# Kernel optimization log

Measured on AMD Instinct MI355X. Metric: run time of the kernel, lower is better.

## Reference

```python
import jax, jax.numpy as jnp
import numpy as np

N_NODES = 50000
N_EDGES = 800000
VOCAB = 15000
IN_FEATS = 128
HIDDEN = 32
HEADS = 4
N_GRAPHS = 64
NEG_SLOPE = 0.2


def setup_inputs() -> dict:
    key = jax.random.key(0)
    ks = jax.random.split(key, 16)
    word_ids = jax.random.randint(ks[0], (N_NODES,), 0, VOCAB)
    edge_src = jax.random.randint(ks[1], (N_EDGES,), 0, N_NODES)
    edge_dst = jax.random.randint(ks[2], (N_EDGES,), 0, N_NODES)
    node_graph_id = jnp.sort(jax.random.randint(ks[3], (N_NODES,), 0, N_GRAPHS))
    y_data = jax.random.uniform(ks[4], (N_GRAPHS,))
    word_embeds = jax.random.normal(ks[5], (VOCAB, IN_FEATS)) * 0.02
    W0 = jax.random.normal(ks[6], (IN_FEATS, HEADS * HIDDEN)) * (1.0 / np.sqrt(IN_FEATS))
    al0 = jax.random.normal(ks[7], (HEADS, HIDDEN)) * 0.1
    ar0 = jax.random.normal(ks[8], (HEADS, HIDDEN)) * 0.1
    W1 = jax.random.normal(ks[9], (HEADS * HIDDEN, HEADS * HIDDEN)) * (1.0 / np.sqrt(HEADS * HIDDEN))
    al1 = jax.random.normal(ks[10], (HEADS, HIDDEN)) * 0.1
    ar1 = jax.random.normal(ks[11], (HEADS, HIDDEN)) * 0.1
    out_w = jax.random.normal(ks[12], (HEADS * HIDDEN, 1)) * (1.0 / np.sqrt(HEADS * HIDDEN))
    out_b = jnp.zeros((1,))
    return {"word_ids": word_ids, "edge_src": edge_src, "edge_dst": edge_dst,
            "node_graph_id": node_graph_id, "y_data": y_data,
            "word_embeds": word_embeds, "W0": W0, "al0": al0, "ar0": ar0,
            "W1": W1, "al1": al1, "ar1": ar1, "out_w": out_w, "out_b": out_b}


def gat_layer(h, src, dst, W, al, ar):
    # h: [N, Fin] -> feat: [N, H, D]
    feat = (h @ W).reshape(N_NODES, HEADS, HIDDEN)
    el = (feat * al[None]).sum(-1)  # [N, H]
    er = (feat * ar[None]).sum(-1)  # [N, H]
    e = jax.nn.leaky_relu(el[src] + er[dst], NEG_SLOPE)  # [E, H]
    # segment softmax over incoming edges of each dst node
    m = jax.ops.segment_max(e, dst, num_segments=N_NODES)
    m = jnp.where(jnp.isfinite(m), m, 0.0)
    ex = jnp.exp(e - m[dst])
    denom = jax.ops.segment_sum(ex, dst, num_segments=N_NODES)
    alpha = ex / (denom[dst] + 1e-10)  # [E, H]
    msg = feat[src] * alpha[:, :, None]  # [E, H, D]
    out = jax.ops.segment_sum(msg, dst, num_segments=N_NODES)  # [N, H, D]
    return jax.nn.elu(out).reshape(N_NODES, HEADS * HIDDEN)


def reference(word_ids, edge_src, edge_dst, node_graph_id, y_data,
              word_embeds, W0, al0, ar0, W1, al1, ar1, out_w, out_b):
    h = word_embeds[word_ids]  # [N, IN_FEATS]
    h = gat_layer(h, edge_src, edge_dst, W0, al0, ar0)
    h = gat_layer(h, edge_src, edge_dst, W1, al1, ar1)
    # per-graph max pooling over nodes
    pooled = jax.ops.segment_max(h, node_graph_id, num_segments=N_GRAPHS)
    pooled = jnp.where(jnp.isfinite(pooled), pooled, 0.0)  # guard empty graphs
    logits = (pooled @ out_w + out_b).reshape(-1)  # [G]
    # BCE with logits (stable)
    loss = jnp.mean(jnp.maximum(logits, 0.0) - logits * y_data
                    + jnp.log1p(jnp.exp(-jnp.abs(logits))))
    y_pred = jax.nn.sigmoid(logits)[:, None]
    return (loss, y_pred)
```

## Files before the change

### kernel.cpp

```cpp
#include <hip/hip_runtime.h>
#include <math.h>

#define N_NODES 50000
#define N_EDGES 800000
#define HEADS 4
#define N_GRAPHS 64
#define NEG_SLOPE 0.2f
#define LOG2E 1.4426950408889634f
#define SCAN_NB 196
#define POOL_CHUNK 50
#define POOL_NB 1000
#define FEAT_NB 782
#define EDGE_Q 200000
#define EDGE_NB 782

typedef __attribute__((ext_vector_type(8))) short bf16x8;
typedef __attribute__((ext_vector_type(4))) float f32x4;

__device__ __forceinline__ unsigned fkey(float f) {
    unsigned u = __float_as_uint(f);
    return (u & 0x80000000u) ? ~u : (u | 0x80000000u);
}
__device__ __forceinline__ float kval(unsigned k) {
    unsigned u = (k & 0x80000000u) ? (k & 0x7FFFFFFFu) : ~k;
    return __uint_as_float(u);
}

__device__ __forceinline__ unsigned short f2bf(float f) {
    unsigned u = __float_as_uint(f);
    u += 0x7FFFu + ((u >> 16) & 1u);
    return (unsigned short)(u >> 16);
}
__device__ __forceinline__ unsigned pack_bf2(float a, float b) {
    return (unsigned)f2bf(a) | ((unsigned)f2bf(b) << 16);
}

__device__ __forceinline__ float elu_fast(float o) {
    float e = exp2f(o * LOG2E) - 1.f;
    return o > 0.f ? o : e;
}


__global__ void hist_kernel(const int* __restrict__ dst, int* __restrict__ deg,
                            int* __restrict__ rank) {
    int i = blockIdx.x * 256 + threadIdx.x;
    if (i >= EDGE_Q) return;
    int e0 = i, e1 = i + EDGE_Q, e2 = i + 2 * EDGE_Q, e3 = i + 3 * EDGE_Q;
    int d0 = dst[e0], d1 = dst[e1], d2 = dst[e2], d3 = dst[e3];
    int r0 = atomicAdd(&deg[d0], 1);
    int r1 = atomicAdd(&deg[d1], 1);
    int r2 = atomicAdd(&deg[d2], 1);
    int r3 = atomicAdd(&deg[d3], 1);
    rank[e0] = r0; rank[e1] = r1; rank[e2] = r2; rank[e3] = r3;
}

__global__ void partial_kernel(const int* __restrict__ deg, int* __restrict__ partial) {
    int t = threadIdx.x, b = blockIdx.x;
    int i = b * 256 + t;
    int v = (i < N_NODES) ? deg[i] : 0;
    #pragma unroll
    for (int off = 1; off < 64; off <<= 1) v += __shfl_xor(v, off, 64);
    __shared__ int wsum[4];
    if ((t & 63) == 0) wsum[t >> 6] = v;
    __syncthreads();
    if (t == 0) partial[b] = wsum[0] + wsum[1] + wsum[2] + wsum[3];
}

__global__ void csr_offsets_kernel(const int* __restrict__ deg, const int* __restrict__ partial,
                                   int* __restrict__ row_start) {
    __shared__ int sb[SCAN_NB];
    __shared__ int wsumA[4];
    __shared__ int wsumB[4];
    int t = threadIdx.x, b = blockIdx.x;
    int lane = t & 63, w = t >> 6;
    {
        int v = (t < SCAN_NB) ? partial[t] : 0;
        int incl = v;
        #pragma unroll
        for (int off = 1; off < 64; off <<= 1) {
            int u = __shfl_up(incl, off, 64);
            if (lane >= off) incl += u;
        }
        if (lane == 63) wsumA[w] = incl;
        __syncthreads();
        int woff = 0;
        #pragma unroll
        for (int k = 0; k < 4; ++k) if (k < w) woff += wsumA[k];
        if (t < SCAN_NB) sb[t] = woff + incl - v;
        __syncthreads();
    }
    int i = b * 256 + t;
    int v = (i < N_NODES) ? deg[i] : 0;
    int incl = v;
    #pragma unroll
    for (int off = 1; off < 64; off <<= 1) {
        int u = __shfl_up(incl, off, 64);
        if (lane >= off) incl += u;
    }
    if (lane == 63) wsumB[w] = incl;
    __syncthreads();
    int woff = sb[b];
    #pragma unroll
    for (int k = 0; k < 4; ++k) if (k < w) woff += wsumB[k];
    int excl = woff + incl - v;
    if (i < N_NODES) row_start[i] = excl;
    else if (i == N_NODES) row_start[i] = excl;
}

__device__ __forceinline__ void scatter_body(int bid, const int* __restrict__ src,
                                             const int* __restrict__ dst,
                                             const int* __restrict__ rank,
                                             const int* __restrict__ row_start,
                                             int* __restrict__ csr_src) {
    int i = bid * 256 + threadIdx.x;
    if (i >= EDGE_Q) return;
    int e0 = i, e1 = i + EDGE_Q, e2 = i + 2 * EDGE_Q, e3 = i + 3 * EDGE_Q;
    int d0 = dst[e0], d1 = dst[e1], d2 = dst[e2], d3 = dst[e3];
    int k0 = rank[e0], k1 = rank[e1], k2 = rank[e2], k3 = rank[e3];
    int s0 = src[e0], s1 = src[e1], s2 = src[e2], s3 = src[e3];
    csr_src[row_start[d0] + k0] = s0;
    csr_src[row_start[d1] + k1] = s1;
    csr_src[row_start[d2] + k2] = s2;
    csr_src[row_start[d3] + k3] = s3;
}


__device__ __forceinline__ void wfrag_body(const float* __restrict__ W,
                                           unsigned* __restrict__ wf, int slot) {
    int f = slot >> 6, l = slot & 63;
    int n = l & 15, q = l >> 4;
    int ct = f >> 2, kq = f & 3;
    int col = 16 * ct + n;
    int k0 = 32 * kq + 8 * q;
    uint4 o;
    o.x = pack_bf2(W[(k0 + 0) * 128 + col], W[(k0 + 1) * 128 + col]);
    o.y = pack_bf2(W[(k0 + 2) * 128 + col], W[(k0 + 3) * 128 + col]);
    o.z = pack_bf2(W[(k0 + 4) * 128 + col], W[(k0 + 5) * 128 + col]);
    o.w = pack_bf2(W[(k0 + 6) * 128 + col], W[(k0 + 7) * 128 + col]);
    ((uint4*)wf)[slot] = o;
}

__global__ void prep_kernel(const float* __restrict__ W0, const float* __restrict__ W1,
                            unsigned* __restrict__ wf0, unsigned* __restrict__ wf1,
                            int* __restrict__ deg, unsigned* __restrict__ pkeys) {
    int b = blockIdx.x, t = threadIdx.x;
    if (b < 8) {
        wfrag_body(W0, wf0, b * 256 + t);
    } else if (b < 16) {
        wfrag_body(W1, wf1, (b - 8) * 256 + t);
    } else if (b < 16 + SCAN_NB) {
        int i = (b - 16) * 256 + t;
        if (i < N_NODES) deg[i] = 0;
    } else {
        int i = (b - 16 - SCAN_NB) * 256 + t;
        if (i < N_GRAPHS * 128) pkeys[i] = 0;
    }
}

template<int IN_BF16>
__device__ __forceinline__ void feat_body(int bid, const void* __restrict__ hin,
                                          const int* __restrict__ wid,
                                          const unsigned* __restrict__ wf,
                                          const float* __restrict__ al,
                                          const float* __restrict__ ar,
                                          unsigned* __restrict__ featb,
                                          float* __restrict__ el, float* __restrict__ er) {
    __shared__ unsigned hl[64 * 68];
    int t = threadIdx.x;
    int n0 = bid * 64;
    if (IN_BF16) {
        const uint4* hb4 = (const uint4*)hin;
        #pragma unroll
        for (int r = 0; r < 4; ++r) {
            int i = t + 256 * r;
            int n = i >> 4, q = i & 15;
            uint4 v = {0u, 0u, 0u, 0u};
            int gn = n0 + n;
            if (gn < N_NODES) v = hb4[(size_t)gn * 16 + q];
            *(uint4*)&hl[n * 68 + q * 4] = v;
        }
    } else {
        const float4* h4 = (const float4*)hin;
        #pragma unroll
        for (int r = 0; r < 8; ++r) {
            int i = t + 256 * r;
            int n = i >> 5, q4 = i & 31;
            float4 v = {0.f, 0.f, 0.f, 0.f};
            int gn = n0 + n;
            if (gn < N_NODES) {
                int row = wid ? wid[gn] : gn;
                v = h4[(size_t)row * 32 + q4];
            }
            hl[n * 68 + q4 * 2]     = pack_bf2(v.x, v.y);
            hl[n * 68 + q4 * 2 + 1] = pack_bf2(v.z, v.w);
        }
    }
    __syncthreads();
    int w = t >> 6, lane = t & 63;
    int col = lane & 15, quad = lane >> 4;
    int nbase = n0 + 16 * w;
    bf16x8 afr[4];
    #pragma unroll
    for (int kq = 0; kq < 4; ++kq)
        afr[kq] = *(const bf16x8*)&hl[(16 * w + col) * 68 + 16 * kq + 4 * quad];
    f32x4 acc[8];
    #pragma unroll
    for (int ct = 0; ct < 8; ++ct) acc[ct] = (f32x4){0.f, 0.f, 0.f, 0.f};
    const uint4* wf4 = (const uint4*)wf;
    #pragma unroll
    for (int ct = 0; ct < 8; ++ct) {
        #pragma unroll
        for (int kq = 0; kq < 4; ++kq) {
            uint4 braw = wf4[(ct * 4 + kq) * 64 + lane];
            bf16x8 bfr = *(const bf16x8*)&braw;
            acc[ct] = __builtin_amdgcn_mfma_f32_16x16x32_bf16(afr[kq], bfr, acc[ct], 0, 0, 0);
        }
    }
    #pragma unroll
    for (int ct = 0; ct < 8; ++ct) {
        #pragma unroll
        for (int reg = 0; reg < 4; ++reg) {
            float v = acc[ct][reg];
            float pv = __shfl_xor(v, 1, 64);
            int node = nbase + quad * 4 + reg;
            if (!(col & 1) && node < N_NODES)
                featb[(size_t)node * 64 + ct * 8 + (col >> 1)] = pack_bf2(v, pv);
        }
    }
    float alv[8], arv[8];
    #pragma unroll
    for (int ct = 0; ct < 8; ++ct) {
        alv[ct] = al[ct * 16 + col];
        arv[ct] = ar[ct * 16 + col];
    }
    #pragma unroll
    for (int reg = 0; reg < 4; ++reg) {
        int node = nbase + quad * 4 + reg;
        #pragma unroll
        for (int hd = 0; hd < 4; ++hd) {
            float pl = acc[2 * hd][reg] * alv[2 * hd] + acc[2 * hd + 1][reg] * alv[2 * hd + 1];
            float pr = acc[2 * hd][reg] * arv[2 * hd] + acc[2 * hd + 1][reg] * arv[2 * hd + 1];
            #pragma unroll
            for (int off = 1; off < 16; off <<= 1) {
                pl += __shfl_xor(pl, off, 64);
                pr += __shfl_xor(pr, off, 64);
            }
            if (col == hd && node < N_NODES) {
                el[node * 4 + hd] = pl * LOG2E;
                er[node * 4 + hd] = pr * LOG2E;
            }
        }
    }
}

template<int IN_BF16>
__global__ __launch_bounds__(256)
void feat_kernel_t(const void* __restrict__ hin, const int* __restrict__ wid,
                   const unsigned* __restrict__ wf,
                   const float* __restrict__ al, const float* __restrict__ ar,
                   unsigned* __restrict__ featb, float* __restrict__ el,
                   float* __restrict__ er) {
    feat_body<IN_BF16>(blockIdx.x, hin, wid, wf, al, ar, featb, el, er);
}

__global__ __launch_bounds__(256)
void scatter_feat0_kernel(const int* __restrict__ src, const int* __restrict__ dst,
                          const int* __restrict__ rank, const int* __restrict__ row_start,
                          int* __restrict__ csr_src,
                          const float* __restrict__ emb, const int* __restrict__ wid,
                          const unsigned* __restrict__ wf0,
                          const float* __restrict__ al0, const float* __restrict__ ar0,
                          unsigned* __restrict__ featb, float* __restrict__ el,
                          float* __restrict__ er) {
    if (blockIdx.x < EDGE_NB) {
        scatter_body(blockIdx.x, src, dst, rank, row_start, csr_src);
    } else {
        feat_body<0>(blockIdx.x - EDGE_NB, emb, wid, wf0, al0, ar0, featb, el, er);
    }
}

template<int OUT_BF16>
__global__ void gat_aggregate_t(const int* __restrict__ row_start, const int* __restrict__ csr_src,
                                const unsigned* __restrict__ featb, const float* __restrict__ el,
                                const float* __restrict__ er, float* __restrict__ houtf,
                                unsigned* __restrict__ houtb) {
    int lane = threadIdx.x & 63;
    int d = blockIdx.x * 4 + (threadIdx.x >> 6);
    int beg = row_start[d], end = row_start[d + 1];
    int eg = lane >> 4;
    int li = lane & 15;
    int hc = li >> 2;
    float er_h = er[d * 4 + hc];
    float a0 = 0.f, a1 = 0.f, a2 = 0.f, a3 = 0.f;
    float a4 = 0.f, a5 = 0.f, a6 = 0.f, a7 = 0.f;
    float dsum = 0.f;
    int b8 = beg + ((end - beg) & ~7);
    for (int base = beg; base < b8; base += 8) {
        int ea = base + eg, eb = base + 4 + eg;
        int sa = csr_src[ea];
        int sb = csr_src[eb];
        float la = el[sa * 4 + hc];
        float lb = el[sb * 4 + hc];
        uint4 pa = *(const uint4*)(featb + (size_t)sa * 64 + li * 4);
        uint4 pb = *(const uint4*)(featb + (size_t)sb * 64 + li * 4);
        float va = la + er_h; va = fmaxf(va, NEG_SLOPE * va);
        float vb = lb + er_h; vb = fmaxf(vb, NEG_SLOPE * vb);
        float xa = exp2f(va), xb = exp2f(vb);
        dsum += xa + xb;
        a0 += __uint_as_float(pa.x << 16) * xa;
        a1 += __uint_as_float(pa.x & 0xFFFF0000u) * xa;
        a2 += __uint_as_float(pa.y << 16) * xa;
        a3 += __uint_as_float(pa.y & 0xFFFF0000u) * xa;
        a4 += __uint_as_float(pa.z << 16) * xa;
        a5 += __uint_as_float(pa.z & 0xFFFF0000u) * xa;
        a6 += __uint_as_float(pa.w << 16) * xa;
        a7 += __uint_as_float(pa.w & 0xFFFF0000u) * xa;
        a0 += __uint_as_float(pb.x << 16) * xb;
        a1 += __uint_as_float(pb.x & 0xFFFF0000u) * xb;
        a2 += __uint_as_float(pb.y << 16) * xb;
        a3 += __uint_as_float(pb.y & 0xFFFF0000u) * xb;
        a4 += __uint_as_float(pb.z << 16) * xb;
        a5 += __uint_as_float(pb.z & 0xFFFF0000u) * xb;
        a6 += __uint_as_float(pb.w << 16) * xb;
        a7 += __uint_as_float(pb.w & 0xFFFF0000u) * xb;
    }
    for (int ee = b8 + eg; ee < end; ee += 4) {
        int s = csr_src[ee];
        float lv = el[s * 4 + hc];
        uint4 pv = *(const uint4*)(featb + (size_t)s * 64 + li * 4);
        float v = lv + er_h; v = fmaxf(v, NEG_SLOPE * v);
        float x = exp2f(v);
        dsum += x;
        a0 += __uint_as_float(pv.x << 16) * x;
        a1 += __uint_as_float(pv.x & 0xFFFF0000u) * x;
        a2 += __uint_as_float(pv.y << 16) * x;
        a3 += __uint_as_float(pv.y & 0xFFFF0000u) * x;
        a4 += __uint_as_float(pv.z << 16) * x;
        a5 += __uint_as_float(pv.z & 0xFFFF0000u) * x;
        a6 += __uint_as_float(pv.w << 16) * x;
        a7 += __uint_as_float(pv.w & 0xFFFF0000u) * x;
    }
    #pragma unroll
    for (int off = 16; off < 64; off <<= 1) {
        a0 += __shfl_xor(a0, off, 64);
        a1 += __shfl_xor(a1, off, 64);
        a2 += __shfl_xor(a2, off, 64);
        a3 += __shfl_xor(a3, off, 64);
        a4 += __shfl_xor(a4, off, 64);
        a5 += __shfl_xor(a5, off, 64);
        a6 += __shfl_xor(a6, off, 64);
        a7 += __shfl_xor(a7, off, 64);
        dsum += __shfl_xor(dsum, off, 64);
    }
    if (eg == 0) {
        float inv = 1.f / (dsum + 1e-10f);
        float o0 = elu_fast(a0 * inv), o1 = elu_fast(a1 * inv);
        float o2 = elu_fast(a2 * inv), o3 = elu_fast(a3 * inv);
        float o4 = elu_fast(a4 * inv), o5 = elu_fast(a5 * inv);
        float o6 = elu_fast(a6 * inv), o7 = elu_fast(a7 * inv);
        if (OUT_BF16) {
            uint4 wv;
            wv.x = pack_bf2(o0, o1);
            wv.y = pack_bf2(o2, o3);
            wv.z = pack_bf2(o4, o5);
            wv.w = pack_bf2(o6, o7);
            ((uint4*)(houtb + (size_t)d * 64))[li] = wv;
        } else {
            float4* op = (float4*)(houtf + (size_t)d * 128);
            float4 w0 = {o0, o1, o2, o3};
            float4 w1 = {o4, o5, o6, o7};
            op[li * 2] = w0;
            op[li * 2 + 1] = w1;
        }
    }
}


__global__ void pool_kernel(const int* __restrict__ gid, const float* __restrict__ h,
                            unsigned* __restrict__ pkeys) {
    int t = threadIdx.x;
    int c = t & 127;
    int par = t >> 7;
    int n0 = blockIdx.x * POOL_CHUNK;
    float m = 0.f;
    int cur_g = -1;
    for (int n = n0 + par; n < n0 + POOL_CHUNK; n += 2) {
        int g = gid[n];
        if (g != cur_g) {
            if (cur_g >= 0) atomicMax(&pkeys[cur_g * 128 + c], fkey(m));
            cur_g = g;
            m = -3.0e38f;
        }
        m = fmaxf(m, h[(size_t)n * 128 + c]);
    }
    if (cur_g >= 0) atomicMax(&pkeys[cur_g * 128 + c], fkey(m));
}

__global__ void logits_final_kernel(const unsigned* __restrict__ pkeys,
                                    const float* __restrict__ w, const float* __restrict__ bptr,
                                    const float* __restrict__ y, float* __restrict__ out) {
    __shared__ float slog[N_GRAPHS];
    int t = threadIdx.x;
    int wv = t >> 6, lane = t & 63;
    float b = bptr[0];
    #pragma unroll
    for (int k = 0; k < 16; ++k) {
        int g = wv * 16 + k;
        float sum = 0.f;
        #pragma unroll
        for (int c0 = 0; c0 < 128; c0 += 64) {
            int c = c0 + lane;
            unsigned kk = pkeys[g * 128 + c];
            float v = (kk == 0u) ? 0.f : kval(kk);
            sum += v * w[c];
        }
        #pragma unroll
        for (int off = 32; off; off >>= 1) sum += __shfl_down(sum, off, 64);
        if (lane == 0) slog[g] = sum + b;
    }
    __syncthreads();
    if (t < N_GRAPHS) {
        float l = slog[t];
        float term = fmaxf(l, 0.f) - l * y[t] + log1pf(expf(-fabsf(l)));
        float s = term;
        #pragma unroll
        for (int off = 32; off; off >>= 1) s += __shfl_down(s, off, 64);
        out[1 + t] = 1.f / (1.f + expf(-l));
        if (t == 0) out[0] = s * (1.f / 64.f);
    }
}

extern "C" void kernel_launch(void* const* d_in, const int* in_sizes, int n_in,
                              void* d_out, int out_size, void* d_ws, size_t ws_size,
                              hipStream_t stream) {
    const int* word_ids  = (const int*)d_in[0];
    const int* esrc      = (const int*)d_in[1];
    const int* edst      = (const int*)d_in[2];
    const int* gid       = (const int*)d_in[3];
    const float* y_data  = (const float*)d_in[4];
    const float* emb     = (const float*)d_in[5];
    const float* W0      = (const float*)d_in[6];
    const float* al0     = (const float*)d_in[7];
    const float* ar0     = (const float*)d_in[8];
    const float* W1      = (const float*)d_in[9];
    const float* al1     = (const float*)d_in[10];
    const float* ar1     = (const float*)d_in[11];
    const float* out_w   = (const float*)d_in[12];
    const float* out_b   = (const float*)d_in[13];
    float* out = (float*)d_out;

    float* ws = (float*)d_ws;
    unsigned* featb  = (unsigned*)ws;
    unsigned* hb     = (unsigned*)(ws + 3200000);
    float*    hout   = ws + 6400000;
    float*    el     = ws + 12800000;
    float*    er     = ws + 13000000;
    int*      row_st = (int*)(ws + 13200000);
    int*      deg    = (int*)(ws + 13250004);
    int*      rank   = (int*)(ws + 13300004);
    int*      csrsrc = (int*)(ws + 14100004);
    int*      partial= (int*)(ws + 14900004);
    unsigned* pkeys  = (unsigned*)(ws + 14900204);
    unsigned* wf0    = (unsigned*)(ws + 14908396);
    unsigned* wf1    = (unsigned*)(ws + 14916588);

    prep_kernel<<<16 + SCAN_NB + 32, 256, 0, stream>>>(W0, W1, wf0, wf1, deg, pkeys);
    hist_kernel<<<EDGE_NB, 256, 0, stream>>>(edst, deg, rank);
    partial_kernel<<<SCAN_NB, 256, 0, stream>>>(deg, partial);
    csr_offsets_kernel<<<SCAN_NB, 256, 0, stream>>>(deg, partial, row_st);

    scatter_feat0_kernel<<<EDGE_NB + FEAT_NB, 256, 0, stream>>>(
        esrc, edst, rank, row_st, csrsrc, emb, word_ids, wf0, al0, ar0, featb, el, er);

    gat_aggregate_t<1><<<12500, 256, 0, stream>>>(row_st, csrsrc, featb, el, er, nullptr, hb);
    feat_kernel_t<1><<<FEAT_NB, 256, 0, stream>>>(hb, nullptr, wf1, al1, ar1, featb, el, er);
    gat_aggregate_t<0><<<12500, 256, 0, stream>>>(row_st, csrsrc, featb, el, er, hout, nullptr);

    pool_kernel<<<POOL_NB, 256, 0, stream>>>(gid, hout, pkeys);
    logits_final_kernel<<<1, 256, 0, stream>>>(pkeys, out_w, out_b, y_data, out);
}
```

Measured before the change: 272.7 us.

## Split layer-0 feature blocks across hist and scatter kernels; unroll aggregate by 16

Half of the layer-0 feature-transform blocks now run inside the histogram kernel, with the other half remaining in the scatter kernel. This spreads the compute work alongside the atomic-bound hist and scatter phases so it overlaps with them. The aggregate loop is also unrolled from 8 to 16 edges per iteration, putting more independent gathers in flight. The wider unroll raises register pressure, and nodes with fewer incoming edges now fall through to the scalar tail loop.

```diff
diff --git a/kernel.cpp b/kernel.cpp
--- a/kernel.cpp
+++ b/kernel.cpp
@@ -11,6 +11,7 @@
 #define POOL_CHUNK 50
 #define POOL_NB 1000
 #define FEAT_NB 782
+#define FEAT_H1 391
 #define EDGE_Q 200000
 #define EDGE_NB 782
 
@@ -41,9 +42,9 @@
 }
 
 
-__global__ void hist_kernel(const int* __restrict__ dst, int* __restrict__ deg,
-                            int* __restrict__ rank) {
-    int i = blockIdx.x * 256 + threadIdx.x;
+__device__ __forceinline__ void hist_body(int bid, const int* __restrict__ dst,
+                                          int* __restrict__ deg, int* __restrict__ rank) {
+    int i = bid * 256 + threadIdx.x;
     if (i >= EDGE_Q) return;
     int e0 = i, e1 = i + EDGE_Q, e2 = i + 2 * EDGE_Q, e3 = i + 3 * EDGE_Q;
     int d0 = dst[e0], d1 = dst[e1], d2 = dst[e2], d3 = dst[e3];
@@ -264,6 +265,21 @@
 }
 
 __global__ __launch_bounds__(256)
+void hist_feat0_kernel(const int* __restrict__ dst, int* __restrict__ deg,
+                       int* __restrict__ rank,
+                       const float* __restrict__ emb, const int* __restrict__ wid,
+                       const unsigned* __restrict__ wf0,
+                       const float* __restrict__ al0, const float* __restrict__ ar0,
+                       unsigned* __restrict__ featb, float* __restrict__ el,
+                       float* __restrict__ er) {
+    if (blockIdx.x < EDGE_NB) {
+        hist_body(blockIdx.x, dst, deg, rank);
+    } else {
+        feat_body<0>(blockIdx.x - EDGE_NB, emb, wid, wf0, al0, ar0, featb, el, er);
+    }
+}
+
+__global__ __launch_bounds__(256)
 void scatter_feat0_kernel(const int* __restrict__ src, const int* __restrict__ dst,
                           const int* __restrict__ rank, const int* __restrict__ row_start,
                           int* __restrict__ csr_src,
@@ -275,7 +291,7 @@
     if (blockIdx.x < EDGE_NB) {
         scatter_body(blockIdx.x, src, dst, rank, row_start, csr_src);
     } else {
-        feat_body<0>(blockIdx.x - EDGE_NB, emb, wid, wf0, al0, ar0, featb, el, er);
+        feat_body<0>(blockIdx.x - EDGE_NB + FEAT_H1, emb, wid, wf0, al0, ar0, featb, el, er);
     }
 }
 
@@ -294,19 +310,28 @@
     float a0 = 0.f, a1 = 0.f, a2 = 0.f, a3 = 0.f;
     float a4 = 0.f, a5 = 0.f, a6 = 0.f, a7 = 0.f;
     float dsum = 0.f;
-    int b8 = beg + ((end - beg) & ~7);
-    for (int base = beg; base < b8; base += 8) {
-        int ea = base + eg, eb = base + 4 + eg;
+    int b16 = beg + ((end - beg) & ~15);
+    for (int base = beg; base < b16; base += 16) {
+        int ea = base + eg, eb = base + 4 + eg, ec = base + 8 + eg, ed = base + 12 + eg;
         int sa = csr_src[ea];
         int sb = csr_src[eb];
+        int sc = csr_src[ec];
+        int sd = csr_src[ed];
         float la = el[sa * 4 + hc];
         float lb = el[sb * 4 + hc];
+        float lc = el[sc * 4 + hc];
+        float ld = el[sd * 4 + hc];
         uint4 pa = *(const uint4*)(featb + (size_t)sa * 64 + li * 4);
         uint4 pb = *(const uint4*)(featb + (size_t)sb * 64 + li * 4);
+        uint4 pc = *(const uint4*)(featb + (size_t)sc * 64 + li * 4);
+        uint4 pd = *(const uint4*)(featb + (size_t)sd * 64 + li * 4);
         float va = la + er_h; va = fmaxf(va, NEG_SLOPE * va);
         float vb = lb + er_h; vb = fmaxf(vb, NEG_SLOPE * vb);
-        float xa = exp2f(va), xb = exp2f(vb);
+        float vc = lc + er_h; vc = fmaxf(vc, NEG_SLOPE * vc);
+        float vd = ld + er_h; vd = fmaxf(vd, NEG_SLOPE * vd);
+        float xa = exp2f(va), xb = exp2f(vb), xc = exp2f(vc), xd = exp2f(vd);
         dsum += xa + xb;
+        dsum += xc + xd;
         a0 += __uint_as_float(pa.x << 16) * xa;
         a1 += __uint_as_float(pa.x & 0xFFFF0000u) * xa;
         a2 += __uint_as_float(pa.y << 16) * xa;
@@ -323,8 +348,24 @@
         a5 += __uint_as_float(pb.z & 0xFFFF0000u) * xb;
         a6 += __uint_as_float(pb.w << 16) * xb;
         a7 += __uint_as_float(pb.w & 0xFFFF0000u) * xb;
-    }
-    for (int ee = b8 + eg; ee < end; ee += 4) {
+        a0 += __uint_as_float(pc.x << 16) * xc;
+        a1 += __uint_as_float(pc.x & 0xFFFF0000u) * xc;
+        a2 += __uint_as_float(pc.y << 16) * xc;
+        a3 += __uint_as_float(pc.y & 0xFFFF0000u) * xc;
+        a4 += __uint_as_float(pc.z << 16) * xc;
+        a5 += __uint_as_float(pc.z & 0xFFFF0000u) * xc;
+        a6 += __uint_as_float(pc.w << 16) * xc;
+        a7 += __uint_as_float(pc.w & 0xFFFF0000u) * xc;
+        a0 += __uint_as_float(pd.x << 16) * xd;
+        a1 += __uint_as_float(pd.x & 0xFFFF0000u) * xd;
+        a2 += __uint_as_float(pd.y << 16) * xd;
+        a3 += __uint_as_float(pd.y & 0xFFFF0000u) * xd;
+        a4 += __uint_as_float(pd.z << 16) * xd;
+        a5 += __uint_as_float(pd.z & 0xFFFF0000u) * xd;
+        a6 += __uint_as_float(pd.w << 16) * xd;
+        a7 += __uint_as_float(pd.w & 0xFFFF0000u) * xd;
+    }
+    for (int ee = b16 + eg; ee < end; ee += 4) {
         int s = csr_src[ee];
         float lv = el[s * 4 + hc];
         uint4 pv = *(const uint4*)(featb + (size_t)s * 64 + li * 4);
@@ -465,11 +506,13 @@
     unsigned* wf1    = (unsigned*)(ws + 14916588);
 
     prep_kernel<<<16 + SCAN_NB + 32, 256, 0, stream>>>(W0, W1, wf0, wf1, deg, pkeys);
-    hist_kernel<<<EDGE_NB, 256, 0, stream>>>(edst, deg, rank);
+
+    hist_feat0_kernel<<<EDGE_NB + FEAT_H1, 256, 0, stream>>>(
+        edst, deg, rank, emb, word_ids, wf0, al0, ar0, featb, el, er);
     partial_kernel<<<SCAN_NB, 256, 0, stream>>>(deg, partial);
     csr_offsets_kernel<<<SCAN_NB, 256, 0, stream>>>(deg, partial, row_st);
 
-    scatter_feat0_kernel<<<EDGE_NB + FEAT_NB, 256, 0, stream>>>(
+    scatter_feat0_kernel<<<EDGE_NB + (FEAT_NB - FEAT_H1), 256, 0, stream>>>(
         esrc, edst, rank, row_st, csrsrc, emb, word_ids, wf0, al0, ar0, featb, el, er);
 
     gat_aggregate_t<1><<<12500, 256, 0, stream>>>(row_st, csrsrc, featb, el, er, nullptr, hb);
```

Measured after the change: 281.2 us. 3.1% more time.

## Fuse graph max-pooling into second GAT aggregation via atomicMax

Applied to the files above, without the earlier changes.

Drops the separate pool kernel and the fp32 layer-2 output buffer. The second aggregation kernel now does an atomicMax of each node's ELU outputs straight into the per-graph pooled keys. This removes a 25.6MB write plus read-back and one launch. In exchange it issues 128 atomics per node into only 64×128 addresses, and because nodes are sorted by graph, many of them collide on the same addresses.

```diff
diff --git a/kernel.cpp b/kernel.cpp
--- a/kernel.cpp
+++ b/kernel.cpp
@@ -8,8 +8,6 @@
 #define NEG_SLOPE 0.2f
 #define LOG2E 1.4426950408889634f
 #define SCAN_NB 196
-#define POOL_CHUNK 50
-#define POOL_NB 1000
 #define FEAT_NB 782
 #define EDGE_Q 200000
 #define EDGE_NB 782
@@ -282,8 +280,8 @@
 template<int OUT_BF16>
 __global__ void gat_aggregate_t(const int* __restrict__ row_start, const int* __restrict__ csr_src,
                                 const unsigned* __restrict__ featb, const float* __restrict__ el,
-                                const float* __restrict__ er, float* __restrict__ houtf,
-                                unsigned* __restrict__ houtb) {
+                                const float* __restrict__ er, const int* __restrict__ gid,
+                                unsigned* __restrict__ pkeys, unsigned* __restrict__ houtb) {
     int lane = threadIdx.x & 63;
     int d = blockIdx.x * 4 + (threadIdx.x >> 6);
     int beg = row_start[d], end = row_start[d + 1];
@@ -366,35 +364,20 @@
             wv.w = pack_bf2(o6, o7);
             ((uint4*)(houtb + (size_t)d * 64))[li] = wv;
         } else {
-            float4* op = (float4*)(houtf + (size_t)d * 128);
-            float4 w0 = {o0, o1, o2, o3};
-            float4 w1 = {o4, o5, o6, o7};
-            op[li * 2] = w0;
-            op[li * 2 + 1] = w1;
-        }
-    }
-}
-
-
-__global__ void pool_kernel(const int* __restrict__ gid, const float* __restrict__ h,
-                            unsigned* __restrict__ pkeys) {
-    int t = threadIdx.x;
-    int c = t & 127;
-    int par = t >> 7;
-    int n0 = blockIdx.x * POOL_CHUNK;
-    float m = 0.f;
-    int cur_g = -1;
-    for (int n = n0 + par; n < n0 + POOL_CHUNK; n += 2) {
-        int g = gid[n];
-        if (g != cur_g) {
-            if (cur_g >= 0) atomicMax(&pkeys[cur_g * 128 + c], fkey(m));
-            cur_g = g;
-            m = -3.0e38f;
-        }
-        m = fmaxf(m, h[(size_t)n * 128 + c]);
-    }
-    if (cur_g >= 0) atomicMax(&pkeys[cur_g * 128 + c], fkey(m));
-}
+            int g = gid[d];
+            unsigned* pk = pkeys + g * 128 + li * 8;
+            atomicMax(&pk[0], fkey(o0));
+            atomicMax(&pk[1], fkey(o1));
+            atomicMax(&pk[2], fkey(o2));
+            atomicMax(&pk[3], fkey(o3));
+            atomicMax(&pk[4], fkey(o4));
+            atomicMax(&pk[5], fkey(o5));
+            atomicMax(&pk[6], fkey(o6));
+            atomicMax(&pk[7], fkey(o7));
+        }
+    }
+}
+
 
 __global__ void logits_final_kernel(const unsigned* __restrict__ pkeys,
                                     const float* __restrict__ w, const float* __restrict__ bptr,
@@ -452,17 +435,16 @@
     float* ws = (float*)d_ws;
     unsigned* featb  = (unsigned*)ws;
     unsigned* hb     = (unsigned*)(ws + 3200000);
-    float*    hout   = ws + 6400000;
-    float*    el     = ws + 12800000;
-    float*    er     = ws + 13000000;
-    int*      row_st = (int*)(ws + 13200000);
-    int*      deg    = (int*)(ws + 13250004);
-    int*      rank   = (int*)(ws + 13300004);
-    int*      csrsrc = (int*)(ws + 14100004);
-    int*      partial= (int*)(ws + 14900004);
-    unsigned* pkeys  = (unsigned*)(ws + 14900204);
-    unsigned* wf0    = (unsigned*)(ws + 14908396);
-    unsigned* wf1    = (unsigned*)(ws + 14916588);
+    float*    el     = ws + 6400000;
+    float*    er     = ws + 6600000;
+    int*      row_st = (int*)(ws + 6800000);
+    int*      deg    = (int*)(ws + 6850004);
+    int*      rank   = (int*)(ws + 6900004);
+    int*      csrsrc = (int*)(ws + 7700004);
+    int*      partial= (int*)(ws + 8500004);
+    unsigned* pkeys  = (unsigned*)(ws + 8500204);
+    unsigned* wf0    = (unsigned*)(ws + 8508396);
+    unsigned* wf1    = (unsigned*)(ws + 8516588);
 
     prep_kernel<<<16 + SCAN_NB + 32, 256, 0, stream>>>(W0, W1, wf0, wf1, deg, pkeys);
     hist_kernel<<<EDGE_NB, 256, 0, stream>>>(edst, deg, rank);
@@ -472,10 +454,9 @@
     scatter_feat0_kernel<<<EDGE_NB + FEAT_NB, 256, 0, stream>>>(
         esrc, edst, rank, row_st, csrsrc, emb, word_ids, wf0, al0, ar0, featb, el, er);
 
-    gat_aggregate_t<1><<<12500, 256, 0, stream>>>(row_st, csrsrc, featb, el, er, nullptr, hb);
+    gat_aggregate_t<1><<<12500, 256, 0, stream>>>(row_st, csrsrc, featb, el, er, nullptr, nullptr, hb);
     feat_kernel_t<1><<<FEAT_NB, 256, 0, stream>>>(hb, nullptr, wf1, al1, ar1, featb, el, er);
-    gat_aggregate_t<0><<<12500, 256, 0, stream>>>(row_st, csrsrc, featb, el, er, hout, nullptr);
-
-    pool_kernel<<<POOL_NB, 256, 0, stream>>>(gid, hout, pkeys);
+    gat_aggregate_t<0><<<12500, 256, 0, stream>>>(row_st, csrsrc, featb, el, er, gid, pkeys, nullptr);
+
     logits_final_kernel<<<1, 256, 0, stream>>>(pkeys, out_w, out_b, y_data, out);
 }
```

New measurement: 631.8 us. +131.7%, slower.
